# Performance work log

Hardware: AMD Instinct MI355X
Metric: run time of the kernel (lower is better)

The kernel has to match this reference:

```python
import jax, jax.numpy as jnp
import numpy as np

# dims: batch B, seq S, model D, query heads H, kv heads KV, head_dim HD, group G
B, S, D = 2, 2048, 2048
H, KV, HD = 16, 4, 128
G = H // KV
THETA = 10000.0


def setup_inputs() -> dict:
    key = jax.random.key(0)
    ks = jax.random.split(key, 5)
    x = jax.random.normal(ks[0], (B, S, D), dtype=jnp.float32)
    # RoPE frequencies (real/imag parts of complex freqs_cis)
    inv_freq = 1.0 / (THETA ** (jnp.arange(0, HD, 2, dtype=jnp.float32) / HD))  # (HD/2,)
    t = jnp.arange(S, dtype=jnp.float32)
    freqs = jnp.outer(t, inv_freq)                      # (S, HD/2)
    freqs_cos = jnp.cos(freqs)
    freqs_sin = jnp.sin(freqs)
    # causal additive mask
    mask = jnp.where(jnp.tril(jnp.ones((S, S), dtype=bool)), 0.0, -1e9).astype(jnp.float32)
    sc = 0.02
    wq = jax.random.normal(ks[1], (D, H * HD), dtype=jnp.float32) * sc
    wk = jax.random.normal(ks[2], (D, KV * HD), dtype=jnp.float32) * sc
    wv = jax.random.normal(ks[3], (D, KV * HD), dtype=jnp.float32) * sc
    wo = jax.random.normal(ks[4], (H * HD, D), dtype=jnp.float32) * sc
    return {"x": x, "freqs_cos": freqs_cos, "freqs_sin": freqs_sin, "mask": mask,
            "wq": wq, "wk": wk, "wv": wv, "wo": wo}


def _apply_rope(x, cos, sin):
    # x: (B, S, nh, HD); cos/sin: (S, HD/2). Interleaved complex rotation.
    xr = x.reshape(*x.shape[:-1], HD // 2, 2)
    xe, xo = xr[..., 0], xr[..., 1]
    c = cos[None, :, None, :]
    s = sin[None, :, None, :]
    out_e = xe * c - xo * s
    out_o = xe * s + xo * c
    return jnp.stack([out_e, out_o], axis=-1).reshape(x.shape)


def reference(x, freqs_cos, freqs_sin, mask, wq, wk, wv, wo):
    q = (x @ wq).reshape(B, S, H, HD)
    k = (x @ wk).reshape(B, S, KV, HD)
    v = (x @ wv).reshape(B, S, KV, HD)
    q = _apply_rope(q, freqs_cos, freqs_sin)
    k = _apply_rope(k, freqs_cos, freqs_sin)
    # GQA: group query heads instead of expanding KV (same math as expand)
    qg = q.reshape(B, S, KV, G, HD)
    scale = jnp.sqrt(jnp.float32(HD))
    scores = jnp.einsum('bqkgd,bskd->bkgqs', qg, k) / scale   # (B,KV,G,S,S)
    scores = scores + mask                                     # broadcast (S,S)
    attn = jax.nn.softmax(scores, axis=-1)
    out = jnp.einsum('bkgqs,bskd->bqkgd', attn, v)             # (B,S,KV,G,HD)
    out = out.reshape(B, S, H * HD)
    return out @ wo
```

## Files before the change

### kernel.cpp

```cpp
#include <hip/hip_runtime.h>
#include <type_traits>

typedef short s8v   __attribute__((ext_vector_type(8)));
typedef float f32x4 __attribute__((ext_vector_type(4)));
typedef float f32x16 __attribute__((ext_vector_type(16)));
typedef unsigned int u32x2 __attribute__((ext_vector_type(2)));
typedef unsigned int u32x4 __attribute__((ext_vector_type(4)));

__device__ __forceinline__ unsigned short f2bf(float f) {
    unsigned int u = __builtin_bit_cast(unsigned int, f);
    u += 0x7FFF + ((u >> 16) & 1);
    return (unsigned short)(u >> 16);
}
__device__ __forceinline__ float bf2f(unsigned short b) {
    unsigned int u = ((unsigned int)b) << 16;
    return __builtin_bit_cast(float, u);
}
__device__ __forceinline__ unsigned int cvtpk(float lo, float hi) {
    unsigned int w;
    asm("v_cvt_pk_bf16_f32 %0, %1, %2" : "=v"(w) : "v"(lo), "v"(hi));
    return w;
}

__device__ __forceinline__ void gload16(const void* g, void* l) {
    __builtin_amdgcn_global_load_lds(
        (const __attribute__((address_space(1))) void*)g,
        (__attribute__((address_space(3))) void*)l, 16, 0, 0);
}

__global__ void conv_bf16(const float* __restrict__ src, unsigned short* __restrict__ dst, int n8) {
    int i = blockIdx.x * blockDim.x + threadIdx.x;
    if (i >= n8) return;
    const f32x4* s4 = (const f32x4*)src;
    f32x4 a = s4[2 * i], b = s4[2 * i + 1];
    s8v o;
    o[0] = (short)f2bf(a[0]); o[1] = (short)f2bf(a[1]);
    o[2] = (short)f2bf(a[2]); o[3] = (short)f2bf(a[3]);
    o[4] = (short)f2bf(b[0]); o[5] = (short)f2bf(b[1]);
    o[6] = (short)f2bf(b[2]); o[7] = (short)f2bf(b[3]);
    *(s8v*)(dst + (size_t)i * 8) = o;
}

__global__ void transpose_conv(const float* __restrict__ src, unsigned short* __restrict__ dst,
                               int K, int N) {
    __shared__ float tile[32][33];
    int n0 = blockIdx.x * 32, k0 = blockIdx.y * 32;
    int tx = threadIdx.x, ty = threadIdx.y;
#pragma unroll
    for (int r = 0; r < 4; ++r)
        tile[ty + r * 8][tx] = src[(size_t)(k0 + ty + r * 8) * N + n0 + tx];
    __syncthreads();
#pragma unroll
    for (int r = 0; r < 4; ++r)
        dst[(size_t)(n0 + ty + r * 8) * K + k0 + tx] = f2bf(tile[tx][ty + r * 8]);
}

__global__ void transpose_conv_qkv(const float* __restrict__ wq, const float* __restrict__ wk,
                                   const float* __restrict__ wv, unsigned short* __restrict__ dst) {
    __shared__ float tile[32][33];
    int n0 = blockIdx.x * 32, k0 = blockIdx.y * 32;
    const float* src; int sc, N;
    if (n0 < 2048)      { src = wq; sc = n0;        N = 2048; }
    else if (n0 < 2560) { src = wk; sc = n0 - 2048; N = 512;  }
    else                { src = wv; sc = n0 - 2560; N = 512;  }
    int tx = threadIdx.x, ty = threadIdx.y;
#pragma unroll
    for (int r = 0; r < 4; ++r)
        tile[ty + r * 8][tx] = src[(size_t)(k0 + ty + r * 8) * N + sc + tx];
    __syncthreads();
#pragma unroll
    for (int r = 0; r < 4; ++r)
        dst[(size_t)(n0 + ty + r * 8) * 2048 + k0 + tx] = f2bf(tile[tx][ty + r * 8]);
}

__global__ void vtrans(const unsigned short* __restrict__ qkv, unsigned short* __restrict__ vt) {
    __shared__ unsigned short t[32][33];
    int s0 = blockIdx.x * 32;
    int c0 = blockIdx.y * 32;
    int tx = threadIdx.x, ty = threadIdx.y;
#pragma unroll
    for (int r = 0; r < 4; ++r)
        t[ty + r * 8][tx] = qkv[(size_t)(s0 + ty + r * 8) * 3072 + 2560 + c0 + tx];
    __syncthreads();
    int b = s0 >> 11, s = s0 & 2047;
    size_t dbase = (size_t)(b * 4 + (c0 >> 7)) * 128 + (c0 & 127);
#pragma unroll
    for (int r = 0; r < 4; ++r)
        vt[(dbase + ty + r * 8) * 2048 + s + tx] = t[tx][ty + r * 8];
}

template <typename CT, bool ROPE>
__global__ __launch_bounds__(256)
void gemm_bt(const unsigned short* __restrict__ A, const unsigned short* __restrict__ BT,
             CT* __restrict__ C, const float* __restrict__ fc, const float* __restrict__ fs,
             int M, int N, int K, int ldc) {
    __shared__ unsigned short As[128 * 64];
    __shared__ unsigned short Bs[128 * 64];
    const int tid = threadIdx.x;
    const int wid = tid >> 6, lane = tid & 63;
    const int l31 = lane & 31, h2 = lane >> 5;
    const int brow = blockIdx.y * 128, bcol = blockIdx.x * 128;
    const int wr = wid >> 1, wc = wid & 1;
    f32x16 acc[2][2] = {};

    for (int kt = 0; kt < K; kt += 64) {
#pragma unroll
        for (int i = 0; i < 4; ++i) {
            int c = i * 256 + tid;
            int row = c >> 3, u = c & 7;
            gload16(A + (size_t)(brow + row) * K + kt + ((u ^ (row & 7)) << 3),
                    As + (size_t)c * 8);
            gload16(BT + (size_t)(bcol + row) * K + kt + ((u ^ (row & 7)) << 3),
                    Bs + (size_t)c * 8);
        }
        __syncthreads();
        s8v a[2][4], b[2][4];
#pragma unroll
        for (int mm = 0; mm < 2; ++mm) {
            int row = wr * 64 + mm * 32 + l31;
#pragma unroll
            for (int ks = 0; ks < 4; ++ks)
                a[mm][ks] = *(const s8v*)(As + (size_t)row * 64 +
                                          (((2 * ks + h2) ^ (row & 7)) << 3));
        }
#pragma unroll
        for (int nn = 0; nn < 2; ++nn) {
            int row = wc * 64 + nn * 32 + l31;
#pragma unroll
            for (int ks = 0; ks < 4; ++ks)
                b[nn][ks] = *(const s8v*)(Bs + (size_t)row * 64 +
                                          (((2 * ks + h2) ^ (row & 7)) << 3));
        }
#pragma unroll
        for (int ks = 0; ks < 4; ++ks)
#pragma unroll
            for (int mm = 0; mm < 2; ++mm)
#pragma unroll
                for (int nn = 0; nn < 2; ++nn)
                    acc[mm][nn] = __builtin_amdgcn_mfma_f32_32x32x16_bf16(
                        a[mm][ks], b[nn][ks], acc[mm][nn], 0, 0, 0);
        __syncthreads();
    }
#pragma unroll
    for (int mm = 0; mm < 2; ++mm)
#pragma unroll
        for (int nn = 0; nn < 2; ++nn)
#pragma unroll
            for (int reg = 0; reg < 16; ++reg) {
                int r = brow + wr * 64 + mm * 32 + (reg & 3) + 8 * (reg >> 2) + 4 * h2;
                int c = bcol + wc * 64 + nn * 32 + l31;
                float v = acc[mm][nn][reg];
                if constexpr (ROPE) {
                    float vp = __shfl_xor(v, 1);
                    if (c < 2560) {
                        int fi = ((r & 2047) << 6) + ((c & 127) >> 1);
                        float cs = fc[fi], sn = fs[fi];
                        v = (l31 & 1) ? (vp * sn + v * cs) : (v * cs - vp * sn);
                    }
                }
                if constexpr (std::is_same<CT, float>::value)
                    C[(size_t)r * ldc + c] = v;
                else
                    C[(size_t)r * ldc + c] = f2bf(v);
            }
}

__global__ __launch_bounds__(256)
void attn_kernel(const unsigned short* __restrict__ qkv,
                 const unsigned short* __restrict__ vtg,
                 unsigned short* __restrict__ out) {
    constexpr int S = 2048;
    __shared__ unsigned short Ks[2][64 * 128];
    __shared__ unsigned short Vs[2][128 * 64];
    const int tid = threadIdx.x, lane = tid & 63, wid = tid >> 6;
    const int l31 = lane & 31, h2 = lane >> 5;
    const int lsw = l31 & 7;
    const int g8 = blockIdx.x & 7;
    const int b = g8 >> 2, kvh = g8 & 3;
    const int qi = 63 - (blockIdx.x >> 3);
    const int h = kvh * 4 + wid;
    const int qw = qi * 32;
    const int qq = qw + l31;
    const size_t rs = 3072;
    const float rscale = 0.08838834764831845f;

    const unsigned short* Qp = qkv + (size_t)(b * S + qw) * rs + h * 128 + h2 * 8;
    const unsigned short* Kbase = qkv + (size_t)(b * S) * rs + 2048 + kvh * 128;
    const unsigned short* Vtg = vtg + (size_t)((b * 4 + kvh) * 128) * S;

    s8v qf[8];
#pragma unroll
    for (int kk = 0; kk < 8; ++kk)
        qf[kk] = *(const s8v*)(Qp + (size_t)l31 * rs + kk * 16);

    f32x16 acc[4] = {};
    float m_run = -1e30f, l_run = 0.f;
    const int nt = (qi >> 1) + 1;

    auto stage = [&](int t, int bufi) {
        const int kb64 = t * 64;
#pragma unroll
        for (int i = 0; i < 4; ++i) {
            int c = i * 256 + tid;
            int key = c >> 4, d8 = c & 15;
            gload16(Kbase + (size_t)(kb64 + key) * rs + ((d8 ^ (key & 7)) << 3),
                    &Ks[bufi][(size_t)c * 8]);
        }
#pragma unroll
        for (int i = 0; i < 4; ++i) {
            int c = i * 256 + tid;
            int d = c >> 3, k8 = c & 7;
            gload16(Vtg + (size_t)d * S + kb64 + ((k8 ^ (d & 7)) << 3),
                    &Vs[bufi][(size_t)c * 8]);
        }
    };

    int cur = 0;
    stage(0, 0);
    __syncthreads();

    for (int t = 0; t < nt; ++t) {
        if (t + 1 < nt) stage(t + 1, cur ^ 1);
        const int kb64 = t * 64;
        const char* Kb = (const char*)&Ks[cur][0];
        const char* Vb = (const char*)&Vs[cur][0];

        s8v kf0[8], kf1[8];
#pragma unroll
        for (int kk = 0; kk < 8; ++kk)
            kf0[kk] = *(const s8v*)(Kb + l31 * 256 + (((2 * kk + h2) ^ lsw) << 4));
#pragma unroll
        for (int kk = 0; kk < 8; ++kk)
            kf1[kk] = *(const s8v*)(Kb + (32 + l31) * 256 + (((2 * kk + h2) ^ lsw) << 4));
        s8v vf[4][4];
#pragma unroll
        for (int kb = 0; kb < 4; ++kb)
#pragma unroll
            for (int dblk = 0; dblk < 4; ++dblk)
                vf[kb][dblk] = *(const s8v*)(Vb + (32 * dblk + l31) * 128 +
                                             (((2 * kb + h2) ^ lsw) << 4));

        f32x16 sacc0 = {}, sacc1 = {};
        __builtin_amdgcn_s_setprio(1);
#pragma unroll
        for (int kk = 0; kk < 8; ++kk)
            sacc0 = __builtin_amdgcn_mfma_f32_32x32x16_bf16(kf0[kk], qf[kk], sacc0, 0, 0, 0);
#pragma unroll
        for (int kk = 0; kk < 8; ++kk)
            sacc1 = __builtin_amdgcn_mfma_f32_32x32x16_bf16(kf1[kk], qf[kk], sacc1, 0, 0, 0);
        __builtin_amdgcn_s_setprio(0);

        float sv[32];
#pragma unroll
        for (int g = 0; g < 2; ++g)
#pragma unroll
            for (int r = 0; r < 16; ++r) {
                int key = kb64 + 32 * g + (r & 3) + 8 * (r >> 2) + 4 * h2;
                float s = (g ? sacc1[r] : sacc0[r]) * rscale;
                sv[g * 16 + r] = (key <= qq) ? s : -1e30f;
            }

        float mx = sv[0];
#pragma unroll
        for (int i = 1; i < 32; ++i) mx = fmaxf(mx, sv[i]);
        mx = fmaxf(mx, __shfl_xor(mx, 32));
        if (!__all(mx - m_run <= 8.f)) {
            float mn = fmaxf(m_run, mx);
            float alpha = __expf(m_run - mn);
            m_run = mn;
            l_run *= alpha;
#pragma unroll
            for (int dblk = 0; dblk < 4; ++dblk)
#pragma unroll
                for (int r = 0; r < 16; ++r) acc[dblk][r] *= alpha;
        }
        float ps = 0.f;
#pragma unroll
        for (int i = 0; i < 32; ++i) {
            float e = __expf(sv[i] - m_run);
            sv[i] = e;
            ps += e;
        }
        ps += __shfl_xor(ps, 32);
        l_run += ps;

        unsigned int pw[4][4];
#pragma unroll
        for (int g = 0; g < 2; ++g) {
            unsigned int w[8];
#pragma unroll
            for (int j = 0; j < 8; ++j)
                w[j] = cvtpk(sv[g * 16 + 2 * j], sv[g * 16 + 2 * j + 1]);
#pragma unroll
            for (int u = 0; u < 2; ++u) {
                unsigned int t0 = (unsigned)__shfl_xor((int)w[4 * u + 0], 32);
                unsigned int t1 = (unsigned)__shfl_xor((int)w[4 * u + 1], 32);
                unsigned int t2 = (unsigned)__shfl_xor((int)w[4 * u + 2], 32);
                unsigned int t3 = (unsigned)__shfl_xor((int)w[4 * u + 3], 32);
                pw[2 * g + u][0] = h2 ? t2 : w[4 * u + 0];
                pw[2 * g + u][1] = h2 ? t3 : w[4 * u + 1];
                pw[2 * g + u][2] = h2 ? w[4 * u + 2] : t0;
                pw[2 * g + u][3] = h2 ? w[4 * u + 3] : t1;
            }
        }

        __builtin_amdgcn_s_setprio(1);
#pragma unroll
        for (int kb = 0; kb < 4; ++kb) {
            u32x4 wv;
            wv[0] = pw[kb][0]; wv[1] = pw[kb][1]; wv[2] = pw[kb][2]; wv[3] = pw[kb][3];
            s8v pf = __builtin_bit_cast(s8v, wv);
#pragma unroll
            for (int dblk = 0; dblk < 4; ++dblk)
                acc[dblk] = __builtin_amdgcn_mfma_f32_32x32x16_bf16(vf[kb][dblk], pf, acc[dblk], 0, 0, 0);
        }
        __builtin_amdgcn_s_setprio(0);

        __syncthreads();
        cur ^= 1;
    }

    float inv = 1.f / l_run;
    unsigned short* Op = out + (size_t)(b * S + qq) * 2048 + h * 128 + 4 * h2;
#pragma unroll
    for (int dblk = 0; dblk < 4; ++dblk)
#pragma unroll
        for (int s = 0; s < 4; ++s) {
            u32x2 wv;
            wv[0] = cvtpk(acc[dblk][4 * s + 0] * inv, acc[dblk][4 * s + 1] * inv);
            wv[1] = cvtpk(acc[dblk][4 * s + 2] * inv, acc[dblk][4 * s + 3] * inv);
            *(u32x2*)(Op + 32 * dblk + 8 * s) = wv;
        }
}

extern "C" void kernel_launch(void* const* d_in, const int* in_sizes, int n_in,
                              void* d_out, int out_size, void* d_ws, size_t ws_size,
                              hipStream_t stream) {
    const float* x  = (const float*)d_in[0];
    const float* fc = (const float*)d_in[1];
    const float* fs = (const float*)d_in[2];
    const float* wq = (const float*)d_in[4];
    const float* wk = (const float*)d_in[5];
    const float* wv = (const float*)d_in[6];
    const float* wo = (const float*)d_in[7];
    float* out = (float*)d_out;

    char* ws = (char*)d_ws;
    unsigned short* xb    = (unsigned short*)ws;
    unsigned short* wqkvT = (unsigned short*)(ws + 16777216);
    unsigned short* woT   = (unsigned short*)(ws + 16777216 + 12582912);
    unsigned short* qkvb  = (unsigned short*)(ws + 16777216 + 12582912 + 8388608);
    unsigned short* attnb = xb;
    unsigned short* vtb   = wqkvT;

    conv_bf16<<<4096, 256, 0, stream>>>(x, xb, 1048576);
    dim3 tb(32, 8);
    transpose_conv_qkv<<<dim3(96, 64), tb, 0, stream>>>(wq, wk, wv, wqkvT);
    transpose_conv<<<dim3(64, 64), tb, 0, stream>>>(wo, woT, 2048, 2048);
    gemm_bt<unsigned short, true><<<dim3(24, 32), 256, 0, stream>>>(
        xb, wqkvT, qkvb, fc, fs, 4096, 3072, 2048, 3072);
    vtrans<<<dim3(128, 16), tb, 0, stream>>>(qkvb, vtb);
    attn_kernel<<<512, 256, 0, stream>>>(qkvb, vtb, attnb);
    gemm_bt<float, false><<<dim3(16, 32), 256, 0, stream>>>(
        attnb, woT, out, nullptr, nullptr, 4096, 2048, 2048, 2048);
}
```

Before: 240.0 us.

## Triple-buffer GEMM tiles with async prefetch and widen block to 128x256

```diff
diff --git a/kernel.cpp b/kernel.cpp
--- a/kernel.cpp
+++ b/kernel.cpp
@@ -90,56 +90,73 @@
 }
 
 template <typename CT, bool ROPE>
-__global__ __launch_bounds__(256)
-void gemm_bt(const unsigned short* __restrict__ A, const unsigned short* __restrict__ BT,
-             CT* __restrict__ C, const float* __restrict__ fc, const float* __restrict__ fs,
-             int M, int N, int K, int ldc) {
-    __shared__ unsigned short As[128 * 64];
-    __shared__ unsigned short Bs[128 * 64];
+__global__ __launch_bounds__(512, 2)
+void gemm_bt2(const unsigned short* __restrict__ A, const unsigned short* __restrict__ BT,
+              CT* __restrict__ C, const float* __restrict__ fc, const float* __restrict__ fs,
+              int K, int ldc) {
+    __shared__ unsigned short As[3][128 * 64];
+    __shared__ unsigned short Bs[3][256 * 64];
     const int tid = threadIdx.x;
     const int wid = tid >> 6, lane = tid & 63;
     const int l31 = lane & 31, h2 = lane >> 5;
-    const int brow = blockIdx.y * 128, bcol = blockIdx.x * 128;
-    const int wr = wid >> 1, wc = wid & 1;
+    const int lsw = l31 & 7;
+    const int brow = blockIdx.y * 128, bcol = blockIdx.x * 256;
+    const int wr = wid >> 2, wc = wid & 3;
+    const int NT = K >> 6;
     f32x16 acc[2][2] = {};
 
-    for (int kt = 0; kt < K; kt += 64) {
-#pragma unroll
-        for (int i = 0; i < 4; ++i) {
-            int c = i * 256 + tid;
-            int row = c >> 3, u = c & 7;
-            gload16(A + (size_t)(brow + row) * K + kt + ((u ^ (row & 7)) << 3),
-                    As + (size_t)c * 8);
-            gload16(BT + (size_t)(bcol + row) * K + kt + ((u ^ (row & 7)) << 3),
-                    Bs + (size_t)c * 8);
-        }
-        __syncthreads();
-        s8v a[2][4], b[2][4];
-#pragma unroll
-        for (int mm = 0; mm < 2; ++mm) {
-            int row = wr * 64 + mm * 32 + l31;
-#pragma unroll
-            for (int ks = 0; ks < 4; ++ks)
-                a[mm][ks] = *(const s8v*)(As + (size_t)row * 64 +
-                                          (((2 * ks + h2) ^ (row & 7)) << 3));
-        }
-#pragma unroll
-        for (int nn = 0; nn < 2; ++nn) {
-            int row = wc * 64 + nn * 32 + l31;
-#pragma unroll
-            for (int ks = 0; ks < 4; ++ks)
-                b[nn][ks] = *(const s8v*)(Bs + (size_t)row * 64 +
-                                          (((2 * ks + h2) ^ (row & 7)) << 3));
-        }
-#pragma unroll
-        for (int ks = 0; ks < 4; ++ks)
+    auto issueA = [&](int t2, int c) {
+        int row = c >> 3, u = c & 7;
+        gload16(A + (size_t)(brow + row) * K + t2 * 64 + ((u ^ (row & 7)) << 3),
+                &As[t2 % 3][(size_t)c * 8]);
+    };
+    auto issueB = [&](int t2, int c) {
+        int row = c >> 3, u = c & 7;
+        gload16(BT + (size_t)(bcol + row) * K + t2 * 64 + ((u ^ (row & 7)) << 3),
+                &Bs[t2 % 3][(size_t)c * 8]);
+    };
+    auto stage = [&](int t2) {
+        issueA(t2, tid); issueA(t2, 512 + tid);
+        issueB(t2, tid); issueB(t2, 512 + tid);
+        issueB(t2, 1024 + tid); issueB(t2, 1536 + tid);
+    };
+
+    stage(0);
+    stage(1);
+
+    for (int t = 0; t < NT; ++t) {
+        if (t < NT - 1) asm volatile("s_waitcnt vmcnt(6)" ::: "memory");
+        else            asm volatile("s_waitcnt vmcnt(0)" ::: "memory");
+        __builtin_amdgcn_s_barrier();
+        __builtin_amdgcn_sched_barrier(0);
+        const unsigned short* Ab = &As[t % 3][0];
+        const unsigned short* Bb = &Bs[t % 3][0];
+        const bool pf = (t + 2 < NT);
+#pragma unroll
+        for (int ks = 0; ks < 4; ++ks) {
+            s8v a[2], b[2];
+#pragma unroll
+            for (int mm = 0; mm < 2; ++mm)
+                a[mm] = *(const s8v*)(Ab + (size_t)(wr * 64 + mm * 32 + l31) * 64 +
+                                      (((2 * ks + h2) ^ lsw) << 3));
+#pragma unroll
+            for (int nn = 0; nn < 2; ++nn)
+                b[nn] = *(const s8v*)(Bb + (size_t)(wc * 64 + nn * 32 + l31) * 64 +
+                                      (((2 * ks + h2) ^ lsw) << 3));
+            if (ks == 0 && pf) {
+                issueA(t + 2, tid); issueA(t + 2, 512 + tid); issueB(t + 2, tid);
+            } else if (ks == 1 && pf) {
+                issueB(t + 2, 512 + tid); issueB(t + 2, 1024 + tid); issueB(t + 2, 1536 + tid);
+            }
+            __builtin_amdgcn_s_setprio(1);
 #pragma unroll
             for (int mm = 0; mm < 2; ++mm)
 #pragma unroll
                 for (int nn = 0; nn < 2; ++nn)
                     acc[mm][nn] = __builtin_amdgcn_mfma_f32_32x32x16_bf16(
-                        a[mm][ks], b[nn][ks], acc[mm][nn], 0, 0, 0);
-        __syncthreads();
+                        a[mm], b[nn], acc[mm][nn], 0, 0, 0);
+            __builtin_amdgcn_s_setprio(0);
+        }
     }
 #pragma unroll
     for (int mm = 0; mm < 2; ++mm)
@@ -357,10 +374,10 @@
     dim3 tb(32, 8);
     transpose_conv_qkv<<<dim3(96, 64), tb, 0, stream>>>(wq, wk, wv, wqkvT);
     transpose_conv<<<dim3(64, 64), tb, 0, stream>>>(wo, woT, 2048, 2048);
-    gemm_bt<unsigned short, true><<<dim3(24, 32), 256, 0, stream>>>(
-        xb, wqkvT, qkvb, fc, fs, 4096, 3072, 2048, 3072);
+    gemm_bt2<unsigned short, true><<<dim3(12, 32), 512, 0, stream>>>(
+        xb, wqkvT, qkvb, fc, fs, 2048, 3072);
     vtrans<<<dim3(128, 16), tb, 0, stream>>>(qkvb, vtb);
     attn_kernel<<<512, 256, 0, stream>>>(qkvb, vtb, attnb);
-    gemm_bt<float, false><<<dim3(16, 32), 256, 0, stream>>>(
-        attnb, woT, out, nullptr, nullptr, 4096, 2048, 2048, 2048);
-}
+    gemm_bt2<float, false><<<dim3(8, 32), 512, 0, stream>>>(
+        attnb, woT, out, nullptr, nullptr, 2048, 2048);
+}
```

Result: slower. 291.0 us (+21.3%).
